# Kernel tuning notes

Measured on AMD Instinct MI355X. Metric: run time of the kernel, lower is better.

The kernel has to match this reference:

```python
import jax, jax.numpy as jnp
import numpy as np

EPS = 1e-06


def _feature_map(x):
    # elu(x) + 1  (elu with alpha=1)
    return jnp.where(x > 0, x + 1.0, jnp.exp(x))


def setup_inputs() -> dict:
    key = jax.random.key(0)
    k1, k2, k3 = jax.random.split(key, 3)
    N, L, S, H, D = 4, 8192, 8192, 8, 64
    q = jax.random.normal(k1, (N, L, H, D), dtype=jnp.float32)
    k = jax.random.normal(k2, (N, S, H, D), dtype=jnp.float32)
    v = jax.random.normal(k3, (N, S, H, D), dtype=jnp.float32)
    q_mask = jnp.ones((N, L), dtype=jnp.float32)
    kv_mask = jnp.ones((N, S), dtype=jnp.float32)
    return {"q": q, "k": k, "v": v, "q_mask": q_mask, "kv_mask": kv_mask}


def reference(q, k, v, q_mask, kv_mask):
    # Linear attention with elu+1 feature map (Katharopoulos et al.)
    qf = _feature_map(q)  # [N, L, H, D]
    kf = _feature_map(k)  # [N, S, H, D]
    qf = q_mask[:, :, None, None] * qf
    kf = kv_mask[:, :, None, None] * kf
    vm = kv_mask[:, :, None, None] * v
    S = v.shape[1]
    # global KV state: [N, H, D, Dv]; v scaled by 1/S for numerical stability
    kv = jnp.einsum('nshd,nshv->nhdv', kf, vm / S)
    # normalizer: einsum('nlhd,nshd->nlh') == q . sum_s(k)
    k_sum = kf.sum(axis=1)  # [N, H, D]
    div = 1.0 / (jnp.einsum('nlhd,nhd->nlh', qf, k_sum) + EPS)
    out = S * jnp.einsum('nlhd,nhdv,nlh->nlhv', qf, kv, div)
    return out
```

## Files before the change

### kernel.cpp

```cpp
#include <hip/hip_runtime.h>
#include <math.h>


#define EPS 1e-6f

static constexpr int Nc = 4;
static constexpr int Lc = 8192;
static constexpr int Sc = 8192;
static constexpr int Hc = 8;
static constexpr int NH = Nc * Hc;
static constexpr int STATE = 64 * 64 + 64;
static constexpr int TS = 32;
static constexpr int TSP = 36;
static constexpr int QSP = 68;
static constexpr int ARRB = 64 * TSP * 2;
static constexpr int BUFB = 4 * ARRB;

typedef __attribute__((ext_vector_type(4))) short short4v;
typedef __attribute__((ext_vector_type(8))) short short8v;
typedef __attribute__((ext_vector_type(4))) float f32x4;

__device__ __forceinline__ float fmap(float x) {
    return x > 0.f ? x + 1.f : __expf(x);
}
__device__ __forceinline__ unsigned short f2bf(float x) {
    unsigned int u = __float_as_uint(x);
    u += 0x7FFFu + ((u >> 16) & 1u);
    return (unsigned short)(u >> 16);
}
__device__ __forceinline__ float bf2f(unsigned short h) {
    return __uint_as_float(((unsigned int)h) << 16);
}
__device__ __forceinline__ short8v ld8(const unsigned short* p) {
    short4v a = *(const short4v*)p;
    short4v b = *(const short4v*)(p + 4);
    return __builtin_shufflevector(a, b, 0, 1, 2, 3, 4, 5, 6, 7);
}
__device__ __forceinline__ unsigned int pack2(unsigned short a, unsigned short b) {
    return (unsigned)a | ((unsigned)b << 16);
}

struct K1Tile {
    float4 k0, k1, v0, v1;
    float m0, m1;
};

__global__ __launch_bounds__(512, 4) void k1_partial(
    const float* __restrict__ kg, const float* __restrict__ vg,
    const float* __restrict__ kv_mask,
    float* __restrict__ partial, int chunks, int sc)
{
    __shared__ __align__(16) unsigned char smem[2 * BUFB];

    const int bid = blockIdx.x;
    const int pair = bid / chunks;
    const int chunk = bid - pair * chunks;
    const int n = pair >> 3;
    const int h = pair & 7;
    const int s0 = chunk * sc;
    const int t = threadIdx.x;
    const int lane = t & 63;
    const int wv = t >> 6;
    const bool producer = (wv < 4);
    const int g = t >> 4;
    const int c4 = (t & 15) * 4;
    const int cw = wv - 4;
    const int row16 = lane & 15;
    const int g8 = (lane >> 4) * 8;

    f32x4 acc[4] = {{0.f,0.f,0.f,0.f},{0.f,0.f,0.f,0.f},
                    {0.f,0.f,0.f,0.f},{0.f,0.f,0.f,0.f}};
    float ksm[4] = {0.f, 0.f, 0.f, 0.f};

    const size_t rowstride = (size_t)Hc * 64;
    const size_t gbase = ((size_t)n * Sc * Hc + h) * 64 + c4;
    const int mbase = n * Sc;

    auto issue = [&](int tile, K1Tile& T) {
        const int s = s0 + tile * TS + 2 * g;
        const size_t be = gbase + (size_t)s * rowstride;
        T.k0 = *(const float4*)(kg + be);
        T.k1 = *(const float4*)(kg + be + rowstride);
        T.v0 = *(const float4*)(vg + be);
        T.v1 = *(const float4*)(vg + be + rowstride);
        T.m0 = kv_mask[mbase + s];
        T.m1 = kv_mask[mbase + s + 1];
    };

    auto convert = [&](const K1Tile& T, int b) {
        unsigned char* base = smem + b * BUFB;
        const float* kep = &T.k0.x;
        const float* kop = &T.k1.x;
        const float* vep = &T.v0.x;
        const float* vop = &T.v1.x;
        #pragma unroll
        for (int j = 0; j < 4; ++j) {
            const int off = ((c4 + j) * TSP + 2 * g) * 2;
            const float fe = T.m0 * fmap(kep[j]);
            const float fo = T.m1 * fmap(kop[j]);
            ksm[j] += fe + fo;
            const unsigned short he = f2bf(fe), ho = f2bf(fo);
            *(unsigned int*)(base + 0 * ARRB + off) = pack2(he, ho);
            *(unsigned int*)(base + 1 * ARRB + off) =
                pack2(f2bf(fe - bf2f(he)), f2bf(fo - bf2f(ho)));
            const float ue = T.m0 * vep[j];
            const float uo = T.m1 * vop[j];
            const unsigned short vhe = f2bf(ue), vho = f2bf(uo);
            *(unsigned int*)(base + 2 * ARRB + off) = pack2(vhe, vho);
            *(unsigned int*)(base + 3 * ARRB + off) =
                pack2(f2bf(ue - bf2f(vhe)), f2bf(uo - bf2f(vho)));
        }
    };

    auto mfma_buf = [&](int b) {
        const unsigned short* kh = (const unsigned short*)(smem + b * BUFB + 0 * ARRB);
        const unsigned short* kl = (const unsigned short*)(smem + b * BUFB + 1 * ARRB);
        const unsigned short* vh = (const unsigned short*)(smem + b * BUFB + 2 * ARRB);
        const unsigned short* vl = (const unsigned short*)(smem + b * BUFB + 3 * ARRB);
        const int arow = (cw * 16 + row16) * TSP + g8;
        const short8v Ah = ld8(kh + arow);
        const short8v Al = ld8(kl + arow);
        #pragma unroll
        for (int bt = 0; bt < 4; ++bt) {
            const int brow = (bt * 16 + row16) * TSP + g8;
            const short8v Bh = ld8(vh + brow);
            const short8v Bl = ld8(vl + brow);
            acc[bt] = __builtin_amdgcn_mfma_f32_16x16x32_bf16(Ah, Bh, acc[bt], 0, 0, 0);
            acc[bt] = __builtin_amdgcn_mfma_f32_16x16x32_bf16(Al, Bh, acc[bt], 0, 0, 0);
            acc[bt] = __builtin_amdgcn_mfma_f32_16x16x32_bf16(Ah, Bl, acc[bt], 0, 0, 0);
        }
    };

    const int NT = sc / TS;
    K1Tile A, B;
    if (producer) issue(0, A);

    for (int tt = 0; tt < NT; tt += 2) {
        if (producer) {
            issue(tt + 1, B);
            convert(A, 0);
        } else if (tt >= 1) {
            mfma_buf(1);
        }
        __syncthreads();
        if (producer) {
            const int nx = (tt + 2 < NT) ? tt + 2 : tt + 1;
            issue(nx, A);
            convert(B, 1);
        } else {
            mfma_buf(0);
        }
        __syncthreads();
    }
    if (!producer) mfma_buf(1);
    __syncthreads();

    float* outp = partial + (size_t)bid * STATE;
    float (*outs)[QSP] = reinterpret_cast<float (*)[QSP]>(smem);
    float* ksb = reinterpret_cast<float*>(smem + BUFB);
    if (!producer) {
        #pragma unroll
        for (int bt = 0; bt < 4; ++bt)
            #pragma unroll
            for (int r = 0; r < 4; ++r)
                outs[cw * 16 + (lane >> 4) * 4 + r][bt * 16 + row16] = acc[bt][r];
    } else {
        *(f32x4*)&ksb[g * 64 + c4] = (f32x4){ksm[0], ksm[1], ksm[2], ksm[3]};
    }
    __syncthreads();

    if (t < 64) {
        float s = 0.f;
        #pragma unroll
        for (int i = 0; i < 16; ++i) s += ksb[i * 64 + t];
        outp[4096 + t] = s;
    }
    #pragma unroll
    for (int p = 0; p < 2; ++p) {
        const int f = t + p * 512;
        const int row = f >> 4;
        const int cc = (f & 15) * 4;
        *(float4*)(outp + row * 64 + cc) = *(const float4*)&outs[row][cc];
    }
}

__global__ __launch_bounds__(256) void k2c_reduce_finalize(
    const float* __restrict__ src, float* __restrict__ dst, int nred)
{
    const int b = blockIdx.x;
    const int pair = b >> 1;
    const int sub = b & 1;
    const int t = threadIdx.x;
    const int ep = sub * 256 + t;
    const int d0 = (ep >> 4) * 2;
    const int c4 = (ep & 15) * 4;

    const float* sbase = src + (size_t)pair * nred * STATE;
    f32x4 a0 = {0.f,0.f,0.f,0.f}, a1 = {0.f,0.f,0.f,0.f};
    #pragma unroll 4
    for (int j = 0; j < nred; ++j) {
        const float* pj = sbase + (size_t)j * STATE;
        a0 += *(const f32x4*)(pj + (size_t)d0 * 64 + c4);
        a1 += *(const f32x4*)(pj + (size_t)(d0 + 1) * 64 + c4);
    }

    unsigned int* dw = (unsigned int*)(dst + (size_t)pair * STATE);
    #pragma unroll
    for (int i = 0; i < 4; ++i) {
        const int w = (c4 + i) * 32 + (d0 >> 1);
        const unsigned short h0 = f2bf(a0[i]), h1 = f2bf(a1[i]);
        dw[w] = pack2(h0, h1);
        dw[2048 + w] = pack2(f2bf(a0[i] - bf2f(h0)), f2bf(a1[i] - bf2f(h1)));
    }

    if (sub == 0 && t < 16) {
        f32x4 a = {0.f,0.f,0.f,0.f};
        #pragma unroll 4
        for (int j = 0; j < nred; ++j)
            a += *(const f32x4*)(sbase + (size_t)j * STATE + 4096 + t * 4);
        *(f32x4*)(dst + (size_t)pair * STATE + 4096 + t * 4) = a;
    }
}

__global__ __launch_bounds__(256, 4) void k3_out(
    const float* __restrict__ qg, const float* __restrict__ state,
    const float* __restrict__ q_mask, float* __restrict__ outg)
{
    __shared__ __align__(16) unsigned short qsp[2][64][QSP];
    __shared__ unsigned short kvt[2][64][QSP];
    __shared__ float ksum[64];
    __shared__ float dinv[64];

    const int nblk = 64;
    const int bid = blockIdx.x;
    const int pair = bid / nblk;
    const int lb = (bid - pair * nblk) * 2;
    const int n = pair >> 3;
    const int h = pair & 7;
    const int t = threadIdx.x;
    const int lane = t & 63;
    const int wv = t >> 6;
    const int row16 = lane & 15;
    const int g8 = (lane >> 4) * 8;

    const unsigned int* sw = (const unsigned int*)(state + (size_t)pair * STATE);
    #pragma unroll
    for (int i = 0; i < 8; ++i) {
        const int w = t + i * 256;
        const int dv = w >> 5;
        const int d2 = (w & 31) * 2;
        *(unsigned int*)&kvt[0][dv][d2] = sw[w];
        *(unsigned int*)&kvt[1][dv][d2] = sw[2048 + w];
    }
    if (t < 64) ksum[t] = ((const float*)state)[(size_t)pair * STATE + 4096 + t];
    __syncthreads();

    for (int tl = 0; tl < 2; ++tl) {
        const int l0 = (lb + tl) * 64;

        #pragma unroll
        for (int p = 0; p < 4; ++p) {
            const int f = t + p * 256;
            const int row = f >> 4;
            const int c4 = (f & 15) * 4;
            const int l = l0 + row;
            const size_t base = ((size_t)(n * Lc + l) * Hc + h) * 64 + c4;
            const float4 qq = *(const float4*)(qg + base);
            const float m = q_mask[n * Lc + l];
            const float q0 = m * fmap(qq.x), q1 = m * fmap(qq.y);
            const float q2 = m * fmap(qq.z), q3 = m * fmap(qq.w);
            const unsigned short h0 = f2bf(q0), h1 = f2bf(q1), h2 = f2bf(q2), h3 = f2bf(q3);
            *(unsigned int*)&qsp[0][row][c4]     = pack2(h0, h1);
            *(unsigned int*)&qsp[0][row][c4 + 2] = pack2(h2, h3);
            *(unsigned int*)&qsp[1][row][c4]     = pack2(f2bf(q0 - bf2f(h0)), f2bf(q1 - bf2f(h1)));
            *(unsigned int*)&qsp[1][row][c4 + 2] = pack2(f2bf(q2 - bf2f(h2)), f2bf(q3 - bf2f(h3)));
            float dp = q0 * ksum[c4] + q1 * ksum[c4 + 1] + q2 * ksum[c4 + 2] + q3 * ksum[c4 + 3];
            dp += __shfl_xor(dp, 1);
            dp += __shfl_xor(dp, 2);
            dp += __shfl_xor(dp, 4);
            dp += __shfl_xor(dp, 8);
            if ((t & 15) == 0) dinv[row] = 1.0f / (dp + EPS);
        }
        __syncthreads();

        f32x4 acc[4] = {{0.f,0.f,0.f,0.f},{0.f,0.f,0.f,0.f},
                        {0.f,0.f,0.f,0.f},{0.f,0.f,0.f,0.f}};
        #pragma unroll
        for (int ks = 0; ks < 2; ++ks) {
            const short8v Ah = ld8(&qsp[0][wv * 16 + row16][ks * 32 + g8]);
            const short8v Al = ld8(&qsp[1][wv * 16 + row16][ks * 32 + g8]);
            #pragma unroll
            for (int bt = 0; bt < 4; ++bt) {
                const short8v Bh = ld8(&kvt[0][bt * 16 + row16][ks * 32 + g8]);
                const short8v Bl = ld8(&kvt[1][bt * 16 + row16][ks * 32 + g8]);
                acc[bt] = __builtin_amdgcn_mfma_f32_16x16x32_bf16(Ah, Bh, acc[bt], 0, 0, 0);
                acc[bt] = __builtin_amdgcn_mfma_f32_16x16x32_bf16(Al, Bh, acc[bt], 0, 0, 0);
                acc[bt] = __builtin_amdgcn_mfma_f32_16x16x32_bf16(Ah, Bl, acc[bt], 0, 0, 0);
            }
        }
        __syncthreads();

        float (*outs)[QSP] = reinterpret_cast<float (*)[QSP]>(&qsp[0][0][0]);
        #pragma unroll
        for (int bt = 0; bt < 4; ++bt) {
            #pragma unroll
            for (int r = 0; r < 4; ++r) {
                const int row = wv * 16 + (lane >> 4) * 4 + r;
                outs[row][bt * 16 + row16] = acc[bt][r] * dinv[row];
            }
        }
        __syncthreads();

        #pragma unroll
        for (int p = 0; p < 4; ++p) {
            const int f = t + p * 256;
            const int row = f >> 4;
            const int c4 = (f & 15) * 4;
            const size_t base = ((size_t)(n * Lc + l0 + row) * Hc + h) * 64 + c4;
            *(float4*)(outg + base) = *(const float4*)&outs[row][c4];
        }
        __syncthreads();
    }
}

extern "C" void kernel_launch(void* const* d_in, const int* in_sizes, int n_in,
                              void* d_out, int out_size, void* d_ws, size_t ws_size,
                              hipStream_t stream)
{
    (void)in_sizes; (void)n_in; (void)out_size;
    const float* q       = (const float*)d_in[0];
    const float* k       = (const float*)d_in[1];
    const float* v       = (const float*)d_in[2];
    const float* q_mask  = (const float*)d_in[3];
    const float* kv_mask = (const float*)d_in[4];
    float* out = (float*)d_out;

    const size_t stBytes  = (size_t)STATE * sizeof(float);
    const size_t finBytes = (size_t)NH * stBytes;

    float* fin = (float*)d_ws;
    float* p1  = (float*)((char*)d_ws + finBytes);

    int chunks = 0;
    for (int c = 32; c >= 8; c >>= 1) {
        if (ws_size >= finBytes + (size_t)NH * c * stBytes) { chunks = c; break; }
    }

    if (chunks >= 8) {
        k1_partial<<<NH * chunks, 512, 0, stream>>>(k, v, kv_mask, p1, chunks, Sc / chunks);
        k2c_reduce_finalize<<<NH * 2, 256, 0, stream>>>(p1, fin, chunks);
    } else {
        k1_partial<<<NH, 512, 0, stream>>>(k, v, kv_mask, p1, 1, Sc);
        k2c_reduce_finalize<<<NH * 2, 256, 0, stream>>>(p1, fin, 1);
    }

    k3_out<<<NH * 64, 256, 0, stream>>>(q, fin, q_mask, out);
}
```

Baseline: 74.75 us.

## Unify k1 producer/consumer waves and give each k3 block more query tiles

The k1 kernel drops its warp-specialized design, where 4 waves converted K/V to split-bf16 in shared memory while 4 other waves ran the MFMAs. It now uses 256 threads that each load, convert, synchronize and then run the MFMAs on the same double-buffered tile, with register prefetch of the next tile. The goal is to cut block size, register and barrier overhead and let more blocks be resident. The cost is that conversion and MFMA work no longer overlap across waves inside a block. Separately, k3 blocks now process 4 query tiles instead of 2, which halves the grid and amortizes the per-block load of the KV state into shared memory.

```diff
diff --git a/kernel.cpp b/kernel.cpp
--- a/kernel.cpp
+++ b/kernel.cpp
@@ -45,7 +45,7 @@
     float m0, m1;
 };
 
-__global__ __launch_bounds__(512, 4) void k1_partial(
+__global__ __launch_bounds__(256, 4) void k1_partial(
     const float* __restrict__ kg, const float* __restrict__ vg,
     const float* __restrict__ kv_mask,
     float* __restrict__ partial, int chunks, int sc)
@@ -59,12 +59,10 @@
     const int h = pair & 7;
     const int s0 = chunk * sc;
     const int t = threadIdx.x;
+    const int g = t >> 4;
+    const int c4 = (t & 15) * 4;
     const int lane = t & 63;
     const int wv = t >> 6;
-    const bool producer = (wv < 4);
-    const int g = t >> 4;
-    const int c4 = (t & 15) * 4;
-    const int cw = wv - 4;
     const int row16 = lane & 15;
     const int g8 = (lane >> 4) * 8;
 
@@ -76,8 +74,8 @@
     const size_t gbase = ((size_t)n * Sc * Hc + h) * 64 + c4;
     const int mbase = n * Sc;
 
-    auto issue = [&](int tile, K1Tile& T) {
-        const int s = s0 + tile * TS + 2 * g;
+    auto issue = [&](int sbase, K1Tile& T) {
+        const int s = s0 + sbase + 2 * g;
         const size_t be = gbase + (size_t)s * rowstride;
         T.k0 = *(const float4*)(kg + be);
         T.k1 = *(const float4*)(kg + be + rowstride);
@@ -87,7 +85,7 @@
         T.m1 = kv_mask[mbase + s + 1];
     };
 
-    auto convert = [&](const K1Tile& T, int b) {
+    auto process = [&](const K1Tile& T, int b) {
         unsigned char* base = smem + b * BUFB;
         const float* kep = &T.k0.x;
         const float* kop = &T.k1.x;
@@ -110,14 +108,13 @@
             *(unsigned int*)(base + 3 * ARRB + off) =
                 pack2(f2bf(ue - bf2f(vhe)), f2bf(uo - bf2f(vho)));
         }
-    };
-
-    auto mfma_buf = [&](int b) {
-        const unsigned short* kh = (const unsigned short*)(smem + b * BUFB + 0 * ARRB);
-        const unsigned short* kl = (const unsigned short*)(smem + b * BUFB + 1 * ARRB);
-        const unsigned short* vh = (const unsigned short*)(smem + b * BUFB + 2 * ARRB);
-        const unsigned short* vl = (const unsigned short*)(smem + b * BUFB + 3 * ARRB);
-        const int arow = (cw * 16 + row16) * TSP + g8;
+        __syncthreads();
+
+        const unsigned short* kh = (const unsigned short*)(base + 0 * ARRB);
+        const unsigned short* kl = (const unsigned short*)(base + 1 * ARRB);
+        const unsigned short* vh = (const unsigned short*)(base + 2 * ARRB);
+        const unsigned short* vl = (const unsigned short*)(base + 3 * ARRB);
+        const int arow = (wv * 16 + row16) * TSP + g8;
         const short8v Ah = ld8(kh + arow);
         const short8v Al = ld8(kl + arow);
         #pragma unroll
@@ -131,56 +128,43 @@
         }
     };
 
-    const int NT = sc / TS;
     K1Tile A, B;
-    if (producer) issue(0, A);
-
-    for (int tt = 0; tt < NT; tt += 2) {
-        if (producer) {
-            issue(tt + 1, B);
-            convert(A, 0);
-        } else if (tt >= 1) {
-            mfma_buf(1);
-        }
-        __syncthreads();
-        if (producer) {
-            const int nx = (tt + 2 < NT) ? tt + 2 : tt + 1;
-            issue(nx, A);
-            convert(B, 1);
-        } else {
-            mfma_buf(0);
-        }
-        __syncthreads();
-    }
-    if (!producer) mfma_buf(1);
+    issue(0, A);
+    for (int sb = 0; sb < sc; sb += 2 * TS) {
+        issue(sb + TS, B);
+        process(A, 0);
+        const int na = (sb + 2 * TS < sc) ? sb + 2 * TS : sb;
+        issue(na, A);
+        process(B, 1);
+    }
     __syncthreads();
 
     float* outp = partial + (size_t)bid * STATE;
     float (*outs)[QSP] = reinterpret_cast<float (*)[QSP]>(smem);
     float* ksb = reinterpret_cast<float*>(smem + BUFB);
-    if (!producer) {
-        #pragma unroll
-        for (int bt = 0; bt < 4; ++bt)
-            #pragma unroll
-            for (int r = 0; r < 4; ++r)
-                outs[cw * 16 + (lane >> 4) * 4 + r][bt * 16 + row16] = acc[bt][r];
-    } else {
-        *(f32x4*)&ksb[g * 64 + c4] = (f32x4){ksm[0], ksm[1], ksm[2], ksm[3]};
-    }
+    #pragma unroll
+    for (int bt = 0; bt < 4; ++bt) {
+        #pragma unroll
+        for (int r = 0; r < 4; ++r) {
+            const int row = wv * 16 + (lane >> 4) * 4 + r;
+            outs[row][bt * 16 + row16] = acc[bt][r];
+        }
+    }
+    *(f32x4*)&ksb[g * 64 + c4] = (f32x4){ksm[0], ksm[1], ksm[2], ksm[3]};
     __syncthreads();
 
-    if (t < 64) {
-        float s = 0.f;
-        #pragma unroll
-        for (int i = 0; i < 16; ++i) s += ksb[i * 64 + t];
-        outp[4096 + t] = s;
-    }
     #pragma unroll
-    for (int p = 0; p < 2; ++p) {
-        const int f = t + p * 512;
+    for (int p = 0; p < 4; ++p) {
+        const int f = t + p * 256;
         const int row = f >> 4;
         const int cc = (f & 15) * 4;
         *(float4*)(outp + row * 64 + cc) = *(const float4*)&outs[row][cc];
+    }
+    if (t < 64) {
+        float s = 0.f;
+        #pragma unroll
+        for (int i = 0; i < 16; ++i) s += ksb[i * 64 + t];
+        outp[4096 + t] = s;
     }
 }
 
@@ -231,10 +215,10 @@
     __shared__ float ksum[64];
     __shared__ float dinv[64];
 
-    const int nblk = 64;
+    const int nblk = 32;
     const int bid = blockIdx.x;
     const int pair = bid / nblk;
-    const int lb = (bid - pair * nblk) * 2;
+    const int lb = (bid - pair * nblk) * 4;
     const int n = pair >> 3;
     const int h = pair & 7;
     const int t = threadIdx.x;
@@ -255,7 +239,7 @@
     if (t < 64) ksum[t] = ((const float*)state)[(size_t)pair * STATE + 4096 + t];
     __syncthreads();
 
-    for (int tl = 0; tl < 2; ++tl) {
+    for (int tl = 0; tl < 4; ++tl) {
         const int l0 = (lb + tl) * 64;
 
         #pragma unroll
@@ -347,12 +331,12 @@
     }
 
     if (chunks >= 8) {
-        k1_partial<<<NH * chunks, 512, 0, stream>>>(k, v, kv_mask, p1, chunks, Sc / chunks);
+        k1_partial<<<NH * chunks, 256, 0, stream>>>(k, v, kv_mask, p1, chunks, Sc / chunks);
         k2c_reduce_finalize<<<NH * 2, 256, 0, stream>>>(p1, fin, chunks);
     } else {
-        k1_partial<<<NH, 512, 0, stream>>>(k, v, kv_mask, p1, 1, Sc);
+        k1_partial<<<NH, 256, 0, stream>>>(k, v, kv_mask, p1, 1, Sc);
         k2c_reduce_finalize<<<NH * 2, 256, 0, stream>>>(p1, fin, 1);
     }
 
-    k3_out<<<NH * 64, 256, 0, stream>>>(q, fin, q_mask, out);
-}
+    k3_out<<<NH * 32, 256, 0, stream>>>(q, fin, q_mask, out);
+}
```

New measurement: 74.41 us (median of 2 runs). Within noise of the previous version (-0.5%).
